# Optimization experiments

Hardware: AMD Instinct MI355X
Metric: run time of the kernel (lower is better)

Reference implementation:

```python
import jax, jax.numpy as jnp
import numpy as np

N = 50000
E = 300000
D_IN = 128
H = 256
D_OUT = 256


def _glorot(key, shape):
    fan_in, fan_out = shape[0], shape[1]
    lim = float(np.sqrt(6.0 / (fan_in + fan_out)))
    return jax.random.uniform(key, shape, jnp.float32, -lim, lim)


def setup_inputs() -> dict:
    key = jax.random.key(0)
    ks = jax.random.split(key, 12)
    x = jax.random.normal(ks[0], (N, D_IN), jnp.float32)
    edge_index = jax.random.randint(ks[1], (2, E), 0, N, jnp.int64)
    return {
        "x": x,
        "edge_index": edge_index,
        "W1": _glorot(ks[2], (D_IN, H)),  "b1": jnp.zeros((H,), jnp.float32),
        "Wg1": _glorot(ks[3], (H, H)),    "bg1": jnp.zeros((H,), jnp.float32),
        "Wg2": _glorot(ks[4], (H, H)),    "bg2": jnp.zeros((H,), jnp.float32),
        "W2": _glorot(ks[5], (H, H)),     "b2": jnp.zeros((H,), jnp.float32),
        "W3": _glorot(ks[6], (H, D_OUT)), "b3": jnp.zeros((D_OUT,), jnp.float32),
    }


def _gcn_conv(h, src, dst, W, b):
    # PyG GCNConv: h' = D^-1/2 (A + I) D^-1/2 (h W) + b, deg counted at target with self-loops
    h = h @ W                                           # [N, H]
    deg = jnp.zeros((N,), h.dtype).at[dst].add(1.0) + 1.0
    dinv = jax.lax.rsqrt(deg)                           # deg^-1/2, [N]
    norm = dinv[src] * dinv[dst]                        # [E]
    msg = h[src] * norm[:, None]                        # gather + scale, [E, H]
    agg = jax.ops.segment_sum(msg, dst, num_segments=N)  # scatter-add
    agg = agg + h * (dinv * dinv)[:, None]              # self-loop contribution (norm = 1/deg)
    return agg + b


def reference(x, edge_index, W1, b1, Wg1, bg1, Wg2, bg2, W2, b2, W3, b3):
    src, dst = edge_index[0], edge_index[1]
    h = jax.nn.relu(x @ W1 + b1)
    h = jax.nn.relu(_gcn_conv(h, src, dst, Wg1, bg1))
    h = jax.nn.relu(_gcn_conv(h, src, dst, Wg2, bg2))
    h = jax.nn.relu(h @ W2 + b2)
    return jax.nn.softmax(h @ W3 + b3, axis=1)
```

## Files before the change

### kernel.cpp

```cpp
#include <hip/hip_runtime.h>
#include <math.h>

#define HDIM 256

typedef float floatx4 __attribute__((ext_vector_type(4)));
typedef __bf16 bf16x8 __attribute__((ext_vector_type(8)));
typedef unsigned short ushortx4 __attribute__((ext_vector_type(4)));
typedef unsigned short ushortx8 __attribute__((ext_vector_type(8)));

#define AS1C(p) ((const __attribute__((address_space(1))) void*)(p))
#define AS3(p)  ((__attribute__((address_space(3))) void*)(p))

__device__ inline unsigned short bf16_rn(float f) {
  unsigned u = __float_as_uint(f);
  return (unsigned short)((u + 0x7FFFu + ((u >> 16) & 1u)) >> 16);
}

__device__ inline void split_f32(float f, unsigned short& h, unsigned short& l) {
  unsigned short hb = bf16_rn(f);
  float hf = __uint_as_float(((unsigned)hb) << 16);
  h = hb;
  l = bf16_rn(f - hf);
}


__global__ __launch_bounds__(256)
void prep_w_staged(const float* __restrict__ W, unsigned short* __restrict__ SH,
                   unsigned short* __restrict__ SL, int K) {
  int idx = blockIdx.x * 256 + threadIdx.x;
  int total = K * 32;
  if (idx >= total) return;
  int chunksPerCb = total >> 1;
  int cb = (idx >= chunksPerCb) ? 1 : 0;
  int rem = idx - cb * chunksPerCb;
  int kt = rem >> 9;
  int chunk = rem & 511;
  int kc = chunk >> 7;
  int col = chunk & 127;
  const float* src = W + (size_t)(kt * 32 + kc * 8) * HDIM + cb * 128 + col;
#pragma unroll
  for (int e = 0; e < 8; ++e) {
    unsigned short h, l;
    split_f32(src[(size_t)e * HDIM], h, l);
    SH[(size_t)idx * 8 + e] = h;
    SL[(size_t)idx * 8 + e] = l;
  }
}


__global__ __launch_bounds__(256)
void split_plane(const float* __restrict__ in, unsigned short* __restrict__ H,
                 unsigned short* __restrict__ L, int total8) {
  int i = blockIdx.x * 256 + threadIdx.x;
  if (i >= total8) return;
  const float4* p = (const float4*)in;
  float4 v0 = p[(size_t)i * 2];
  float4 v1 = p[(size_t)i * 2 + 1];
  float f[8] = {v0.x, v0.y, v0.z, v0.w, v1.x, v1.y, v1.z, v1.w};
  ushortx8 hh, ll;
#pragma unroll
  for (int e = 0; e < 8; ++e) {
    unsigned short h, l;
    split_f32(f[e], h, l);
    hh[e] = h;
    ll[e] = l;
  }
  ((ushortx8*)H)[i] = hh;
  ((ushortx8*)L)[i] = ll;
}


__global__ __launch_bounds__(256)
void deg_count_kernel(const int* __restrict__ ei, int* __restrict__ deg, int E) {
  int e = blockIdx.x * 256 + threadIdx.x;
  if (e < E) atomicAdd(&deg[ei[E + e]], 1);
}

__global__ __launch_bounds__(256)
void dinv_kernel(const int* __restrict__ deg, float* __restrict__ dinv, int n) {
  int i = blockIdx.x * 256 + threadIdx.x;
  if (i < n) dinv[i] = 1.0f / sqrtf((float)deg[i] + 1.0f);
}

__global__ __launch_bounds__(256)
void block_sum_kernel(const int* __restrict__ deg, int* __restrict__ bsum, int n) {
  __shared__ int sm[256];
  int t = threadIdx.x;
  int idx = blockIdx.x * 256 + t;
  sm[t] = (idx < n) ? deg[idx] : 0;
  __syncthreads();
  for (int off = 128; off > 0; off >>= 1) {
    if (t < off) sm[t] += sm[t + off];
    __syncthreads();
  }
  if (t == 0) bsum[blockIdx.x] = sm[0];
}

__global__ __launch_bounds__(256)
void scan_bsums_kernel(const int* __restrict__ bsum, int* __restrict__ boff,
                       int* __restrict__ rowptr, int nb, int n) {
  __shared__ int sm[256];
  int t = threadIdx.x;
  int v = (t < nb) ? bsum[t] : 0;
  sm[t] = v;
  __syncthreads();
  for (int off = 1; off < 256; off <<= 1) {
    int a = (t >= off) ? sm[t - off] : 0;
    __syncthreads();
    sm[t] += a;
    __syncthreads();
  }
  if (t < nb) boff[t] = sm[t] - v;
  if (t == 255) rowptr[n] = sm[255];
}

__global__ __launch_bounds__(256)
void scan_final_kernel(const int* __restrict__ deg, const int* __restrict__ boff,
                       int* __restrict__ rowptr, int* __restrict__ cursor, int n) {
  __shared__ int sm[256];
  int t = threadIdx.x;
  int idx = blockIdx.x * 256 + t;
  int v = (idx < n) ? deg[idx] : 0;
  sm[t] = v;
  __syncthreads();
  for (int off = 1; off < 256; off <<= 1) {
    int a = (t >= off) ? sm[t - off] : 0;
    __syncthreads();
    sm[t] += a;
    __syncthreads();
  }
  int excl = sm[t] - v + boff[blockIdx.x];
  if (idx < n) { rowptr[idx] = excl; cursor[idx] = excl; }
}

__global__ __launch_bounds__(256)
void fill_csr_kernel(const int* __restrict__ ei, const float* __restrict__ dinv,
                     int* __restrict__ cursor, int* __restrict__ col,
                     float* __restrict__ wsrc, int E) {
  int e = blockIdx.x * 256 + threadIdx.x;
  if (e < E) {
    int s = ei[e];
    int d = ei[E + e];
    int p = atomicAdd(&cursor[d], 1);
    col[p] = s;
    wsrc[p] = dinv[s];
  }
}


template<bool BIAS, bool RELU, bool SPLIT_OUT>
__global__ __launch_bounds__(256, 2)
void mfma_gemm_p(const unsigned short* __restrict__ AH, const unsigned short* __restrict__ AL,
                 const unsigned short* __restrict__ SWH, const unsigned short* __restrict__ SWL,
                 const float* __restrict__ bias,
                 float* __restrict__ C, unsigned short* __restrict__ CH,
                 unsigned short* __restrict__ CL, int M, int K) {
  __shared__ __align__(16) unsigned short AsH[2][4096];
  __shared__ __align__(16) unsigned short AsL[2][4096];
  __shared__ __align__(16) unsigned short BsH[2][4096];
  __shared__ __align__(16) unsigned short BsL[2][4096];

  const int tid = threadIdx.x;
  const int w = tid >> 6;
  const int l = tid & 63;
  const int l15 = l & 15;
  const int quad = l >> 4;
  const int wm = w & 1;
  const int wn = w >> 1;
  const int bm = blockIdx.y * 128;
  const int bn = blockIdx.x * 128;
  const int ktc = K >> 5;

  floatx4 acc[4][4];
#pragma unroll
  for (int i = 0; i < 4; ++i)
#pragma unroll
    for (int j = 0; j < 4; ++j) acc[i][j] = (floatx4){0.f, 0.f, 0.f, 0.f};

  auto stage = [&](int kt, int buf) {
#pragma unroll
    for (int i = 0; i < 2; ++i) {
      int L = i * 256 + tid;
      int row = L >> 2;
      int p = L & 3;
      int kc = p ^ (row & 3) ^ ((row >> 2) & 3);
      int grow = bm + row;
      if (grow > M - 1) grow = M - 1;
      const unsigned short* gH = AH + (size_t)grow * K + kt * 32 + kc * 8;
      const unsigned short* gL = AL + (size_t)grow * K + kt * 32 + kc * 8;
      __builtin_amdgcn_global_load_lds(AS1C(gH), AS3(&AsH[buf][(i * 256 + w * 64) * 8]), 16, 0, 0);
      __builtin_amdgcn_global_load_lds(AS1C(gL), AS3(&AsL[buf][(i * 256 + w * 64) * 8]), 16, 0, 0);
    }
    size_t wb = ((size_t)(blockIdx.x * ktc + kt)) * 4096;
#pragma unroll
    for (int j = 0; j < 2; ++j) {
      int c = j * 256 + tid;
      __builtin_amdgcn_global_load_lds(AS1C(SWH + wb + (size_t)c * 8),
                                       AS3(&BsH[buf][(j * 256 + w * 64) * 8]), 16, 0, 0);
      __builtin_amdgcn_global_load_lds(AS1C(SWL + wb + (size_t)c * 8),
                                       AS3(&BsL[buf][(j * 256 + w * 64) * 8]), 16, 0, 0);
    }
  };

  stage(0, 0);
  __syncthreads();
  int cur = 0;

#pragma unroll 1
  for (int kt = 0; kt < ktc; ++kt) {
    if (kt + 1 < ktc) stage(kt + 1, cur ^ 1);

    bf16x8 aH[4], aL[4];
#pragma unroll
    for (int fi = 0; fi < 4; ++fi) {
      int r = wm * 64 + fi * 16 + l15;
      int sw = quad ^ (r & 3) ^ ((r >> 2) & 3);
      aH[fi] = *(const bf16x8*)&AsH[cur][(r * 4 + sw) * 8];
      aL[fi] = *(const bf16x8*)&AsL[cur][(r * 4 + sw) * 8];
    }
#pragma unroll
    for (int fj = 0; fj < 4; ++fj) {
      int colL = wn * 64 + fj * 16 + l15;
      int cidx = quad * 128 + colL;
      bf16x8 bh = *(const bf16x8*)&BsH[cur][cidx * 8];
      bf16x8 bl = *(const bf16x8*)&BsL[cur][cidx * 8];
#pragma unroll
      for (int fi = 0; fi < 4; ++fi) {
        floatx4 t = acc[fi][fj];
        t = __builtin_amdgcn_mfma_f32_16x16x32_bf16(aH[fi], bl, t, 0, 0, 0);
        t = __builtin_amdgcn_mfma_f32_16x16x32_bf16(aL[fi], bh, t, 0, 0, 0);
        t = __builtin_amdgcn_mfma_f32_16x16x32_bf16(aH[fi], bh, t, 0, 0, 0);
        acc[fi][fj] = t;
      }
    }

    __syncthreads();
    cur ^= 1;
  }

  float bcol[4];
#pragma unroll
  for (int fj = 0; fj < 4; ++fj)
    bcol[fj] = BIAS ? bias[bn + wn * 64 + fj * 16 + l15] : 0.f;

#pragma unroll
  for (int fi = 0; fi < 4; ++fi) {
    int rb = bm + wm * 64 + fi * 16 + quad * 4;
#pragma unroll
    for (int r = 0; r < 4; ++r) {
      int row = rb + r;
      if (row < M) {
        size_t base = (size_t)row * HDIM + bn + wn * 64 + l15;
        if (SPLIT_OUT) {
#pragma unroll
          for (int fj = 0; fj < 4; ++fj) {
            float v = acc[fi][fj][r] + bcol[fj];
            if (RELU) v = fmaxf(v, 0.f);
            unsigned short h, lo;
            split_f32(v, h, lo);
            CH[base + fj * 16] = h;
            CL[base + fj * 16] = lo;
          }
        } else {
#pragma unroll
          for (int fj = 0; fj < 4; ++fj) {
            float v = acc[fi][fj][r] + bcol[fj];
            if (RELU) v = fmaxf(v, 0.f);
            C[base + fj * 16] = v;
          }
        }
      }
    }
  }
}


__global__ __launch_bounds__(512, 4)
void mfma_gemm_softmax(const unsigned short* __restrict__ AH, const unsigned short* __restrict__ AL,
                       const unsigned short* __restrict__ SWH, const unsigned short* __restrict__ SWL,
                       const float* __restrict__ bias, float* __restrict__ out, int M, int K) {
  __shared__ __align__(16) unsigned short AsH[4096];
  __shared__ __align__(16) unsigned short AsL[4096];
  __shared__ __align__(16) unsigned short BsH[8192];
  __shared__ __align__(16) unsigned short BsL[8192];
  __shared__ float smax[128 * 4];
  __shared__ float ssum[128 * 4];

  const int tid = threadIdx.x;
  const int w = tid >> 6;
  const int l = tid & 63;
  const int l15 = l & 15;
  const int quad = l >> 4;
  const int wm = w & 1;
  const int wn = w >> 1;
  const int bm = blockIdx.x * 128;
  const int ktc = K >> 5;
  const int chunksPerCb = ktc * 512;

  floatx4 acc[4][4];
#pragma unroll
  for (int i = 0; i < 4; ++i)
#pragma unroll
    for (int j = 0; j < 4; ++j) acc[i][j] = (floatx4){0.f, 0.f, 0.f, 0.f};

  for (int kt = 0; kt < ktc; ++kt) {
    __syncthreads();

    {
      int L = tid;
      int row = L >> 2;
      int p = L & 3;
      int kc = p ^ (row & 3) ^ ((row >> 2) & 3);
      int grow = bm + row;
      if (grow > M - 1) grow = M - 1;
      const unsigned short* gH = AH + (size_t)grow * K + kt * 32 + kc * 8;
      const unsigned short* gL = AL + (size_t)grow * K + kt * 32 + kc * 8;
      __builtin_amdgcn_global_load_lds(AS1C(gH), AS3(&AsH[(w * 64) * 8]), 16, 0, 0);
      __builtin_amdgcn_global_load_lds(AS1C(gL), AS3(&AsL[(w * 64) * 8]), 16, 0, 0);
    }
#pragma unroll
    for (int j = 0; j < 2; ++j) {
      int pos = j * 512 + w * 64 + l;
      int kc = pos >> 8;
      int within = pos & 255;
      int cb = within >> 7;
      int colL = within & 127;
      size_t gi = (size_t)cb * chunksPerCb + (size_t)kt * 512 + kc * 128 + colL;
      __builtin_amdgcn_global_load_lds(AS1C(SWH + gi * 8),
                                       AS3(&BsH[(j * 512 + w * 64) * 8]), 16, 0, 0);
      __builtin_amdgcn_global_load_lds(AS1C(SWL + gi * 8),
                                       AS3(&BsL[(j * 512 + w * 64) * 8]), 16, 0, 0);
    }

    __syncthreads();

    bf16x8 aH[4], aL[4];
#pragma unroll
    for (int fi = 0; fi < 4; ++fi) {
      int r = wm * 64 + fi * 16 + l15;
      int sw = quad ^ (r & 3) ^ ((r >> 2) & 3);
      aH[fi] = *(const bf16x8*)&AsH[(r * 4 + sw) * 8];
      aL[fi] = *(const bf16x8*)&AsL[(r * 4 + sw) * 8];
    }
#pragma unroll
    for (int fj = 0; fj < 4; ++fj) {
      int colG = wn * 64 + fj * 16 + l15;
      int cidx = quad * 256 + colG;
      bf16x8 bh = *(const bf16x8*)&BsH[cidx * 8];
      bf16x8 bl = *(const bf16x8*)&BsL[cidx * 8];
#pragma unroll
      for (int fi = 0; fi < 4; ++fi) {
        floatx4 t = acc[fi][fj];
        t = __builtin_amdgcn_mfma_f32_16x16x32_bf16(aH[fi], bl, t, 0, 0, 0);
        t = __builtin_amdgcn_mfma_f32_16x16x32_bf16(aL[fi], bh, t, 0, 0, 0);
        t = __builtin_amdgcn_mfma_f32_16x16x32_bf16(aH[fi], bh, t, 0, 0, 0);
        acc[fi][fj] = t;
      }
    }
  }

  float bcol[4];
#pragma unroll
  for (int fj = 0; fj < 4; ++fj)
    bcol[fj] = bias[wn * 64 + fj * 16 + l15];

#pragma unroll
  for (int fi = 0; fi < 4; ++fi) {
#pragma unroll
    for (int r = 0; r < 4; ++r) {
      float mv = -3.4e38f;
#pragma unroll
      for (int fj = 0; fj < 4; ++fj) mv = fmaxf(mv, acc[fi][fj][r] + bcol[fj]);
#pragma unroll
      for (int off = 1; off < 16; off <<= 1) mv = fmaxf(mv, __shfl_xor(mv, off));
      int row = wm * 64 + fi * 16 + quad * 4 + r;
      if (l15 == 0) smax[row * 4 + wn] = mv;
    }
  }
  __syncthreads();

#pragma unroll
  for (int fi = 0; fi < 4; ++fi) {
#pragma unroll
    for (int r = 0; r < 4; ++r) {
      int row = wm * 64 + fi * 16 + quad * 4 + r;
      float gm = fmaxf(fmaxf(smax[row * 4 + 0], smax[row * 4 + 1]),
                       fmaxf(smax[row * 4 + 2], smax[row * 4 + 3]));
      float s = 0.f;
#pragma unroll
      for (int fj = 0; fj < 4; ++fj) {
        float p = expf(acc[fi][fj][r] + bcol[fj] - gm);
        acc[fi][fj][r] = p;
        s += p;
      }
#pragma unroll
      for (int off = 1; off < 16; off <<= 1) s += __shfl_xor(s, off);
      if (l15 == 0) ssum[row * 4 + wn] = s;
    }
  }
  __syncthreads();

#pragma unroll
  for (int fi = 0; fi < 4; ++fi) {
#pragma unroll
    for (int r = 0; r < 4; ++r) {
      int row = wm * 64 + fi * 16 + quad * 4 + r;
      int grow = bm + row;
      if (grow < M) {
        float inv = 1.0f / (ssum[row * 4 + 0] + ssum[row * 4 + 1] +
                            ssum[row * 4 + 2] + ssum[row * 4 + 3]);
        float* Cp = out + (size_t)grow * HDIM + wn * 64 + l15;
#pragma unroll
        for (int fj = 0; fj < 4; ++fj) Cp[fj * 16] = acc[fi][fj][r] * inv;
      }
    }
  }
}


__global__ __launch_bounds__(256)
void aggregate_b(const float* __restrict__ t, const float* __restrict__ dinv,
                 const int* __restrict__ rowptr, const int* __restrict__ col,
                 const float* __restrict__ wsrc, const float* __restrict__ bias,
                 unsigned short* __restrict__ OH, unsigned short* __restrict__ OL, int n) {
  int gw = (int)((blockIdx.x * 256 + threadIdx.x) >> 6);
  int lane = threadIdx.x & 63;
  if (gw >= n) return;
  float di = dinv[gw];
  float4 v = ((const float4*)(t + (size_t)gw * HDIM))[lane];
  float ss = di * di;
  float a0 = v.x * ss, a1 = v.y * ss, a2 = v.z * ss, a3 = v.w * ss;
  int e0 = rowptr[gw], e1 = rowptr[gw + 1];

  for (int base = e0; base < e1; base += 8) {
    int cs[8];
    float wv[8];
#pragma unroll
    for (int i = 0; i < 8; ++i) {
      int e = base + i;
      if (e > e1 - 1) e = e1 - 1;
      cs[i] = col[e];
      wv[i] = wsrc[e];
    }
    float wg[8];
#pragma unroll
    for (int i = 0; i < 8; ++i)
      wg[i] = (base + i < e1) ? wv[i] * di : 0.f;
    float4 rw[8];
#pragma unroll
    for (int i = 0; i < 8; ++i)
      rw[i] = ((const float4*)(t + (size_t)cs[i] * HDIM))[lane];
#pragma unroll
    for (int i = 0; i < 8; ++i) {
      a0 = fmaf(rw[i].x, wg[i], a0);
      a1 = fmaf(rw[i].y, wg[i], a1);
      a2 = fmaf(rw[i].z, wg[i], a2);
      a3 = fmaf(rw[i].w, wg[i], a3);
    }
  }

  float4 bb = ((const float4*)bias)[lane];
  float r0 = fmaxf(a0 + bb.x, 0.f);
  float r1 = fmaxf(a1 + bb.y, 0.f);
  float r2 = fmaxf(a2 + bb.z, 0.f);
  float r3 = fmaxf(a3 + bb.w, 0.f);
  unsigned short h0, h1, h2, h3, l0, l1, l2, l3;
  split_f32(r0, h0, l0);
  split_f32(r1, h1, l1);
  split_f32(r2, h2, l2);
  split_f32(r3, h3, l3);
  ((ushortx4*)(OH + (size_t)gw * HDIM))[lane] = (ushortx4){h0, h1, h2, h3};
  ((ushortx4*)(OL + (size_t)gw * HDIM))[lane] = (ushortx4){l0, l1, l2, l3};
}


extern "C" void kernel_launch(void* const* d_in, const int* in_sizes, int n_in,
                              void* d_out, int out_size, void* d_ws, size_t ws_size,
                              hipStream_t stream) {
  const float* x   = (const float*)d_in[0];
  const int*   ei  = (const int*)d_in[1];
  const float* W1  = (const float*)d_in[2];
  const float* b1  = (const float*)d_in[3];
  const float* Wg1 = (const float*)d_in[4];
  const float* bg1 = (const float*)d_in[5];
  const float* Wg2 = (const float*)d_in[6];
  const float* bg2 = (const float*)d_in[7];
  const float* W2  = (const float*)d_in[8];
  const float* b2  = (const float*)d_in[9];
  const float* W3  = (const float*)d_in[10];
  const float* b3  = (const float*)d_in[11];
  float* out = (float*)d_out;

  const int K1 = in_sizes[2] / HDIM;
  const int N  = in_sizes[0] / K1;
  const int E  = in_sizes[1] / 2;

  char* w = (char*)d_ws;
  auto alloc = [&](size_t bytes) -> char* {
    char* p = w;
    w += (bytes + 255) & ~(size_t)255;
    return p;
  };
  unsigned short* PH = (unsigned short*)alloc((size_t)N * HDIM * 2);
  unsigned short* PL = (unsigned short*)alloc((size_t)N * HDIM * 2);
  float* dinv   = (float*)alloc((size_t)N * sizeof(float));
  int*   deg    = (int*)alloc((size_t)N * sizeof(int));
  int*   rowptr = (int*)alloc((size_t)(N + 1) * sizeof(int));
  int*   cursor = (int*)alloc((size_t)N * sizeof(int));
  int*   col    = (int*)alloc((size_t)E * sizeof(int));
  float* wcsr   = (float*)alloc((size_t)E * sizeof(float));
  const int nb  = (N + 255) / 256;
  int*   bsum   = (int*)alloc((size_t)nb * sizeof(int));
  int*   boff   = (int*)alloc((size_t)nb * sizeof(int));
  unsigned short* W1sH  = (unsigned short*)alloc((size_t)HDIM * K1 * 2);
  unsigned short* W1sL  = (unsigned short*)alloc((size_t)HDIM * K1 * 2);
  unsigned short* Wg1sH = (unsigned short*)alloc((size_t)HDIM * HDIM * 2);
  unsigned short* Wg1sL = (unsigned short*)alloc((size_t)HDIM * HDIM * 2);
  unsigned short* Wg2sH = (unsigned short*)alloc((size_t)HDIM * HDIM * 2);
  unsigned short* Wg2sL = (unsigned short*)alloc((size_t)HDIM * HDIM * 2);
  unsigned short* W2sH  = (unsigned short*)alloc((size_t)HDIM * HDIM * 2);
  unsigned short* W2sL  = (unsigned short*)alloc((size_t)HDIM * HDIM * 2);
  unsigned short* W3sH  = (unsigned short*)alloc((size_t)HDIM * HDIM * 2);
  unsigned short* W3sL  = (unsigned short*)alloc((size_t)HDIM * HDIM * 2);

  unsigned short* XH = (unsigned short*)out;
  unsigned short* XL = XH + (size_t)N * K1;
  unsigned short* QH = (unsigned short*)out;
  unsigned short* QL = QH + (size_t)N * HDIM;

  const int ge = (E + 255) / 256;
  const int gn = (N + 255) / 256;

  prep_w_staged<<<(K1 * 32 + 255) / 256, 256, 0, stream>>>(W1, W1sH, W1sL, K1);
  prep_w_staged<<<(HDIM * 32 + 255) / 256, 256, 0, stream>>>(Wg1, Wg1sH, Wg1sL, HDIM);
  prep_w_staged<<<(HDIM * 32 + 255) / 256, 256, 0, stream>>>(Wg2, Wg2sH, Wg2sL, HDIM);
  prep_w_staged<<<(HDIM * 32 + 255) / 256, 256, 0, stream>>>(W2, W2sH, W2sL, HDIM);
  prep_w_staged<<<(HDIM * 32 + 255) / 256, 256, 0, stream>>>(W3, W3sH, W3sL, HDIM);

  hipMemsetAsync(deg, 0, (size_t)N * sizeof(int), stream);
  deg_count_kernel<<<ge, 256, 0, stream>>>(ei, deg, E);
  dinv_kernel<<<gn, 256, 0, stream>>>(deg, dinv, N);
  block_sum_kernel<<<nb, 256, 0, stream>>>(deg, bsum, N);
  scan_bsums_kernel<<<1, 256, 0, stream>>>(bsum, boff, rowptr, nb, N);
  scan_final_kernel<<<nb, 256, 0, stream>>>(deg, boff, rowptr, cursor, N);
  fill_csr_kernel<<<ge, 256, 0, stream>>>(ei, dinv, cursor, col, wcsr, E);

  dim3 ggrid(2, (N + 127) / 128);
  const int gagg = (N + 3) / 4;
  const int gfuse = (N + 127) / 128;
  const int tot8 = N * K1 / 8;

  split_plane<<<(tot8 + 255) / 256, 256, 0, stream>>>(x, XH, XL, tot8);
  mfma_gemm_p<true, true, true><<<ggrid, 256, 0, stream>>>(XH, XL, W1sH, W1sL, b1, nullptr, PH, PL, N, K1);
  mfma_gemm_p<false, false, false><<<ggrid, 256, 0, stream>>>(PH, PL, Wg1sH, Wg1sL, nullptr, out, nullptr, nullptr, N, HDIM);
  aggregate_b<<<gagg, 256, 0, stream>>>(out, dinv, rowptr, col, wcsr, bg1, PH, PL, N);
  mfma_gemm_p<false, false, false><<<ggrid, 256, 0, stream>>>(PH, PL, Wg2sH, Wg2sL, nullptr, out, nullptr, nullptr, N, HDIM);
  aggregate_b<<<gagg, 256, 0, stream>>>(out, dinv, rowptr, col, wcsr, bg2, PH, PL, N);
  mfma_gemm_p<true, true, true><<<ggrid, 256, 0, stream>>>(PH, PL, W2sH, W2sL, b2, nullptr, QH, QL, N, HDIM);
  mfma_gemm_softmax<<<gfuse, 512, 0, stream>>>(QH, QL, W3sH, W3sL, b3, out, N, HDIM);
}
```

Measured before the change: 433.2 us.

## Widen GEMM block to full 256 columns with 512 threads, drop double buffering

The split-bf16 GEMM now runs 512-thread blocks that each cover a 128x256 output tile, so every A row tile is loaded once instead of once per column half. The weight staging is re-indexed to pull both column blocks per k-step. Double-buffered LDS staging is replaced by a single buffer with syncs before and after each load, which saves LDS but exposes global load latency that was previously overlapped. Launch bounds change to 512 threads with a higher occupancy hint.

New measurement: 403.8 us. 6.8% less time.

```diff
diff --git a/kernel.cpp b/kernel.cpp
--- a/kernel.cpp
+++ b/kernel.cpp
@@ -149,16 +149,16 @@
 
 
 template<bool BIAS, bool RELU, bool SPLIT_OUT>
-__global__ __launch_bounds__(256, 2)
+__global__ __launch_bounds__(512, 4)
 void mfma_gemm_p(const unsigned short* __restrict__ AH, const unsigned short* __restrict__ AL,
                  const unsigned short* __restrict__ SWH, const unsigned short* __restrict__ SWL,
                  const float* __restrict__ bias,
                  float* __restrict__ C, unsigned short* __restrict__ CH,
                  unsigned short* __restrict__ CL, int M, int K) {
-  __shared__ __align__(16) unsigned short AsH[2][4096];
-  __shared__ __align__(16) unsigned short AsL[2][4096];
-  __shared__ __align__(16) unsigned short BsH[2][4096];
-  __shared__ __align__(16) unsigned short BsL[2][4096];
+  __shared__ __align__(16) unsigned short AsH[4096];
+  __shared__ __align__(16) unsigned short AsL[4096];
+  __shared__ __align__(16) unsigned short BsH[8192];
+  __shared__ __align__(16) unsigned short BsL[8192];
 
   const int tid = threadIdx.x;
   const int w = tid >> 6;
@@ -167,9 +167,9 @@
   const int quad = l >> 4;
   const int wm = w & 1;
   const int wn = w >> 1;
-  const int bm = blockIdx.y * 128;
-  const int bn = blockIdx.x * 128;
+  const int bm = blockIdx.x * 128;
   const int ktc = K >> 5;
+  const int chunksPerCb = ktc * 512;
 
   floatx4 acc[4][4];
 #pragma unroll
@@ -177,10 +177,11 @@
 #pragma unroll
     for (int j = 0; j < 4; ++j) acc[i][j] = (floatx4){0.f, 0.f, 0.f, 0.f};
 
-  auto stage = [&](int kt, int buf) {
-#pragma unroll
-    for (int i = 0; i < 2; ++i) {
-      int L = i * 256 + tid;
+  for (int kt = 0; kt < ktc; ++kt) {
+    __syncthreads();
+
+    {
+      int L = tid;
       int row = L >> 2;
       int p = L & 3;
       int kc = p ^ (row & 3) ^ ((row >> 2) & 3);
@@ -188,42 +189,39 @@
       if (grow > M - 1) grow = M - 1;
       const unsigned short* gH = AH + (size_t)grow * K + kt * 32 + kc * 8;
       const unsigned short* gL = AL + (size_t)grow * K + kt * 32 + kc * 8;
-      __builtin_amdgcn_global_load_lds(AS1C(gH), AS3(&AsH[buf][(i * 256 + w * 64) * 8]), 16, 0, 0);
-      __builtin_amdgcn_global_load_lds(AS1C(gL), AS3(&AsL[buf][(i * 256 + w * 64) * 8]), 16, 0, 0);
-    }
-    size_t wb = ((size_t)(blockIdx.x * ktc + kt)) * 4096;
+      __builtin_amdgcn_global_load_lds(AS1C(gH), AS3(&AsH[(w * 64) * 8]), 16, 0, 0);
+      __builtin_amdgcn_global_load_lds(AS1C(gL), AS3(&AsL[(w * 64) * 8]), 16, 0, 0);
+    }
 #pragma unroll
     for (int j = 0; j < 2; ++j) {
-      int c = j * 256 + tid;
-      __builtin_amdgcn_global_load_lds(AS1C(SWH + wb + (size_t)c * 8),
-                                       AS3(&BsH[buf][(j * 256 + w * 64) * 8]), 16, 0, 0);
-      __builtin_amdgcn_global_load_lds(AS1C(SWL + wb + (size_t)c * 8),
-                                       AS3(&BsL[buf][(j * 256 + w * 64) * 8]), 16, 0, 0);
-    }
-  };
-
-  stage(0, 0);
-  __syncthreads();
-  int cur = 0;
-
-#pragma unroll 1
-  for (int kt = 0; kt < ktc; ++kt) {
-    if (kt + 1 < ktc) stage(kt + 1, cur ^ 1);
+      int pos = j * 512 + w * 64 + l;
+      int kc = pos >> 8;
+      int within = pos & 255;
+      int cb = within >> 7;
+      int colL = within & 127;
+      size_t gi = (size_t)cb * chunksPerCb + (size_t)kt * 512 + kc * 128 + colL;
+      __builtin_amdgcn_global_load_lds(AS1C(SWH + gi * 8),
+                                       AS3(&BsH[(j * 512 + w * 64) * 8]), 16, 0, 0);
+      __builtin_amdgcn_global_load_lds(AS1C(SWL + gi * 8),
+                                       AS3(&BsL[(j * 512 + w * 64) * 8]), 16, 0, 0);
+    }
+
+    __syncthreads();
 
     bf16x8 aH[4], aL[4];
 #pragma unroll
     for (int fi = 0; fi < 4; ++fi) {
       int r = wm * 64 + fi * 16 + l15;
       int sw = quad ^ (r & 3) ^ ((r >> 2) & 3);
-      aH[fi] = *(const bf16x8*)&AsH[cur][(r * 4 + sw) * 8];
-      aL[fi] = *(const bf16x8*)&AsL[cur][(r * 4 + sw) * 8];
+      aH[fi] = *(const bf16x8*)&AsH[(r * 4 + sw) * 8];
+      aL[fi] = *(const bf16x8*)&AsL[(r * 4 + sw) * 8];
     }
 #pragma unroll
     for (int fj = 0; fj < 4; ++fj) {
-      int colL = wn * 64 + fj * 16 + l15;
-      int cidx = quad * 128 + colL;
-      bf16x8 bh = *(const bf16x8*)&BsH[cur][cidx * 8];
-      bf16x8 bl = *(const bf16x8*)&BsL[cur][cidx * 8];
+      int colG = wn * 64 + fj * 16 + l15;
+      int cidx = quad * 256 + colG;
+      bf16x8 bh = *(const bf16x8*)&BsH[cidx * 8];
+      bf16x8 bl = *(const bf16x8*)&BsL[cidx * 8];
 #pragma unroll
       for (int fi = 0; fi < 4; ++fi) {
         floatx4 t = acc[fi][fj];
@@ -233,15 +231,12 @@
         acc[fi][fj] = t;
       }
     }
-
-    __syncthreads();
-    cur ^= 1;
   }
 
   float bcol[4];
 #pragma unroll
   for (int fj = 0; fj < 4; ++fj)
-    bcol[fj] = BIAS ? bias[bn + wn * 64 + fj * 16 + l15] : 0.f;
+    bcol[fj] = BIAS ? bias[wn * 64 + fj * 16 + l15] : 0.f;
 
 #pragma unroll
   for (int fi = 0; fi < 4; ++fi) {
@@ -250,7 +245,7 @@
     for (int r = 0; r < 4; ++r) {
       int row = rb + r;
       if (row < M) {
-        size_t base = (size_t)row * HDIM + bn + wn * 64 + l15;
+        size_t base = (size_t)row * HDIM + wn * 64 + l15;
         if (SPLIT_OUT) {
 #pragma unroll
           for (int fj = 0; fj < 4; ++fj) {
@@ -545,17 +540,16 @@
   scan_final_kernel<<<nb, 256, 0, stream>>>(deg, boff, rowptr, cursor, N);
   fill_csr_kernel<<<ge, 256, 0, stream>>>(ei, dinv, cursor, col, wcsr, E);
 
-  dim3 ggrid(2, (N + 127) / 128);
+  const int g128 = (N + 127) / 128;
   const int gagg = (N + 3) / 4;
-  const int gfuse = (N + 127) / 128;
   const int tot8 = N * K1 / 8;
 
   split_plane<<<(tot8 + 255) / 256, 256, 0, stream>>>(x, XH, XL, tot8);
-  mfma_gemm_p<true, true, true><<<ggrid, 256, 0, stream>>>(XH, XL, W1sH, W1sL, b1, nullptr, PH, PL, N, K1);
-  mfma_gemm_p<false, false, false><<<ggrid, 256, 0, stream>>>(PH, PL, Wg1sH, Wg1sL, nullptr, out, nullptr, nullptr, N, HDIM);
+  mfma_gemm_p<true, true, true><<<g128, 512, 0, stream>>>(XH, XL, W1sH, W1sL, b1, nullptr, PH, PL, N, K1);
+  mfma_gemm_p<false, false, false><<<g128, 512, 0, stream>>>(PH, PL, Wg1sH, Wg1sL, nullptr, out, nullptr, nullptr, N, HDIM);
   aggregate_b<<<gagg, 256, 0, stream>>>(out, dinv, rowptr, col, wcsr, bg1, PH, PL, N);
-  mfma_gemm_p<false, false, false><<<ggrid, 256, 0, stream>>>(PH, PL, Wg2sH, Wg2sL, nullptr, out, nullptr, nullptr, N, HDIM);
+  mfma_gemm_p<false, false, false><<<g128, 512, 0, stream>>>(PH, PL, Wg2sH, Wg2sL, nullptr, out, nullptr, nullptr, N, HDIM);
   aggregate_b<<<gagg, 256, 0, stream>>>(out, dinv, rowptr, col, wcsr, bg2, PH, PL, N);
-  mfma_gemm_p<true, true, true><<<ggrid, 256, 0, stream>>>(PH, PL, W2sH, W2sL, b2, nullptr, QH, QL, N, HDIM);
-  mfma_gemm_softmax<<<gfuse, 512, 0, stream>>>(QH, QL, W3sH, W3sL, b3, out, N, HDIM);
-}
+  mfma_gemm_p<true, true, true><<<g128, 512, 0, stream>>>(PH, PL, W2sH, W2sL, b2, nullptr, QH, QL, N, HDIM);
+  mfma_gemm_softmax<<<g128, 512, 0, stream>>>(QH, QL, W3sH, W3sL, b3, out, N, HDIM);
+}
```
